# Optimization experiments

Measured on AMD Instinct MI355X. Metric: run time of the kernel, lower is better.

Reference implementation:

```python
import jax, jax.numpy as jnp
import numpy as np

N_NODES = 65536
N_GRAPHS = 32
NODES_PER_GRAPH = 2048
N_EDGES = 1048576
F_IN, H1, H2, OUT = 16, 64, 64, 12


def gcn_conv(x, src, dst, W, b, num_nodes):
    """PyG GCNConv: out = D^{-1/2} (A+I) D^{-1/2} X W + b."""
    loop = jnp.arange(num_nodes, dtype=src.dtype)
    s = jnp.concatenate([src, loop])  # sources incl. self-loops
    d = jnp.concatenate([dst, loop])  # targets incl. self-loops
    deg = jax.ops.segment_sum(jnp.ones_like(d, dtype=x.dtype), d, num_segments=num_nodes)
    dinv = jnp.where(deg > 0, jax.lax.rsqrt(deg), 0.0)
    norm = dinv[s] * dinv[d]  # [E+N]
    h = x @ W  # [N, H]
    msg = h[s] * norm[:, None]  # [E+N, H] -- dominant memory traffic
    return jax.ops.segment_sum(msg, d, num_segments=num_nodes) + b


def setup_inputs() -> dict:
    key = jax.random.key(0)
    k = jax.random.split(key, 8)
    x = jax.random.normal(k[0], (N_NODES, F_IN), dtype=jnp.float32)
    edge_index = jax.random.randint(k[1], (2, N_EDGES), 0, N_NODES, dtype=jnp.int32)
    batch = jnp.repeat(jnp.arange(N_GRAPHS, dtype=jnp.int32), NODES_PER_GRAPH)
    s1 = 1.0 / np.sqrt(F_IN)
    s2 = 1.0 / np.sqrt(H1)
    s3 = 1.0 / np.sqrt(H2 * NODES_PER_GRAPH)
    W1 = jax.random.uniform(k[2], (F_IN, H1), jnp.float32, -s1, s1)
    b1 = jnp.zeros((H1,), jnp.float32)
    W2 = jax.random.uniform(k[3], (H1, H2), jnp.float32, -s2, s2)
    b2 = jnp.zeros((H2,), jnp.float32)
    Wfc = jax.random.uniform(k[4], (H2 * NODES_PER_GRAPH, OUT), jnp.float32, -s3, s3)
    bfc = jax.random.uniform(k[5], (OUT,), jnp.float32, -s3, s3)
    return {"x": x, "edge_index": edge_index, "batch": batch,
            "W1": W1, "b1": b1, "W2": W2, "b2": b2, "Wfc": Wfc, "bfc": bfc}


def reference(x, edge_index, batch, W1, b1, W2, b2, Wfc, bfc):
    src, dst = edge_index[0], edge_index[1]
    h = gcn_conv(x, src, dst, W1, b1, N_NODES)
    h = jnp.tanh(h)  # act1 (dropout rate 0 -> identity)
    h = gcn_conv(h, src, dst, W2, b2, N_NODES)
    h = jnp.tanh(h)  # act2
    # batch is sorted with exactly NODES_PER_GRAPH nodes per graph, so the
    # per-graph masked concat is a reshape: [G, P*H2]
    h_concat = h.reshape(N_GRAPHS, NODES_PER_GRAPH * H2)
    return h_concat @ Wfc + bfc
```

## Files before the change

kernel.cpp:

```cpp
#include <hip/hip_runtime.h>
#include <hip/hip_fp16.h>

#define N_NODES 65536
#define N_EDGES 1048576
#define F_IN    16
#define H       64
#define N_GRAPHS 32
#define NPG     2048
#define OUT_F   12
#define KPG     (NPG * H)
#define CAP     4864
#define NPB     16


__global__ __launch_bounds__(256) void init_kernel(int* __restrict__ gCursor,
                                                   const float* __restrict__ bfc,
                                                   float* __restrict__ out) {
    int t = threadIdx.x;
    gCursor[t] = t * CAP;
    for (int i = t; i < N_GRAPHS * OUT_F; i += 256) out[i] = bfc[i % OUT_F];
}

__global__ __launch_bounds__(256) void binA_kernel(const int* __restrict__ src,
                                                   const int* __restrict__ dst,
                                                   int* __restrict__ gCursor,
                                                   unsigned int* __restrict__ binned) {
    __shared__ int hist[256];
    __shared__ int sc[256];
    __shared__ int bnd[257];
    __shared__ int lcur[256];
    __shared__ int blkBase[256];
    __shared__ unsigned int staged[4096];
    int t = threadIdx.x;
    hist[t] = 0; lcur[t] = 0;
    __syncthreads();
    int e0 = blockIdx.x * 4096;
    unsigned int rec[16];
#pragma unroll
    for (int i = 0; i < 16; i++) {
        int e = e0 + i * 256 + t;
        unsigned int s = (unsigned int)src[e];
        unsigned int d = (unsigned int)dst[e];
        rec[i] = s | (d << 16);
        atomicAdd(&hist[d >> 8], 1);
    }
    __syncthreads();
    int cnt = hist[t];
    if (cnt) blkBase[t] = atomicAdd(&gCursor[t], cnt);
    sc[t] = cnt;
    __syncthreads();
    for (int off = 1; off < 256; off <<= 1) {
        int v = (t >= off) ? sc[t - off] : 0;
        __syncthreads();
        sc[t] += v;
        __syncthreads();
    }
    bnd[t] = sc[t] - cnt;
    if (t == 255) bnd[256] = 4096;
    __syncthreads();
#pragma unroll
    for (int i = 0; i < 16; i++) {
        int b = rec[i] >> 24;
        int p = bnd[b] + atomicAdd(&lcur[b], 1);
        staged[p] = rec[i];
    }
    __syncthreads();
    for (int i = t; i < 4096; i += 256) {
        int lo = 0;
#pragma unroll
        for (int s = 128; s > 0; s >>= 1)
            if (bnd[lo + s] <= i) lo += s;
        binned[blkBase[lo] + (i - bnd[lo])] = staged[i];
    }
}

__global__ __launch_bounds__(256) void binB_g1_kernel(const unsigned int* __restrict__ binned,
                                                      const int* __restrict__ gCursor,
                                                      const float* __restrict__ x,
                                                      int2* __restrict__ rowinfo,
                                                      unsigned short* __restrict__ nbr,
                                                      __half2* __restrict__ g1h) {
    __shared__ int hist[256];
    __shared__ int sc[256];
    __shared__ int off[256];
    __shared__ int cur[256];
    __shared__ unsigned short outS[8192];
    int b = blockIdx.x, t = threadIdx.x;
    int base = b * CAP;
    int cnt  = gCursor[b] - base;
    hist[t] = 0; cur[t] = 0;
    __syncthreads();
    for (int i = t; i < cnt; i += 256) {
        unsigned int r = binned[base + i];
        atomicAdd(&hist[(r >> 16) & 255], 1);
    }
    __syncthreads();
    int c = hist[t];
    sc[t] = c;
    __syncthreads();
    for (int o = 1; o < 256; o <<= 1) {
        int v = (t >= o) ? sc[t - o] : 0;
        __syncthreads();
        sc[t] += v;
        __syncthreads();
    }
    off[t] = sc[t] - c;
    int nd = (b << 8) + t;
    float dv = rsqrtf((float)(c + 1));
    rowinfo[nd] = make_int2(base + sc[t] - c, c);
    {
        const float4* xr = (const float4*)(x + (size_t)nd * F_IN);
        float4 x0 = xr[0], x1 = xr[1], x2 = xr[2], x3 = xr[3];
        __half2* gr = g1h + nd * 8;
        gr[0] = __floats2half2_rn(x0.x * dv, x0.y * dv);
        gr[1] = __floats2half2_rn(x0.z * dv, x0.w * dv);
        gr[2] = __floats2half2_rn(x1.x * dv, x1.y * dv);
        gr[3] = __floats2half2_rn(x1.z * dv, x1.w * dv);
        gr[4] = __floats2half2_rn(x2.x * dv, x2.y * dv);
        gr[5] = __floats2half2_rn(x2.z * dv, x2.w * dv);
        gr[6] = __floats2half2_rn(x3.x * dv, x3.y * dv);
        gr[7] = __floats2half2_rn(x3.z * dv, x3.w * dv);
    }
    __syncthreads();
    for (int i = t; i < cnt; i += 256) {
        unsigned int r = binned[base + i];
        int n = (r >> 16) & 255;
        int p = off[n] + atomicAdd(&cur[n], 1);
        outS[p] = (unsigned short)(r & 0xFFFF);
    }
    __syncthreads();
    for (int i = t; i < cnt; i += 256) nbr[base + i] = outS[i];
}

__device__ __forceinline__ void add8(float* acc, float4 q) {
    union { float4 f; __half2 h[4]; } u; u.f = q;
#pragma unroll
    for (int c = 0; c < 4; c++) {
        float2 p = __half22float2(u.h[c]);
        acc[2 * c]     += p.x;
        acc[2 * c + 1] += p.y;
    }
}
__device__ __forceinline__ void add4(float* acc, float2 q) {
    union { float2 f; __half2 h[2]; } u; u.f = q;
    float2 p0 = __half22float2(u.h[0]);
    float2 p1 = __half22float2(u.h[1]);
    acc[0] += p0.x; acc[1] += p0.y; acc[2] += p1.x; acc[3] += p1.y;
}

__global__ __launch_bounds__(256) void agg1_gemm1_kernel(const __half2* __restrict__ g1h,
                                                         const int2* __restrict__ rowinfo,
                                                         const unsigned short* __restrict__ nbr,
                                                         const float* __restrict__ W1,
                                                         const float* __restrict__ b1,
                                                         __half* __restrict__ g2h) {
    const float2* g1v = (const float2*)g1h;
    __shared__ float Ws[F_IN * H];
    __shared__ float bs[H];
    int t = threadIdx.x;
    for (int i = t; i < F_IN * H; i += 256) Ws[i] = W1[i];
    if (t < H) bs[t] = b1[t];
    __syncthreads();
    int lane = t & 63;
    int w    = t >> 6;
    int f4   = lane & 3;
    int sub  = lane >> 2;
    int v    = blockIdx.x * NPB + w;
    int2 ri  = rowinfo[v];
    int nb   = (int)nbr[ri.x + lane];
#pragma unroll 1
    for (int it = 0; it < NPB / 4; ++it) {
        int vc = v;
        int r0 = ri.x, er = ri.y;
        int nbc = nb;
        float2 sq = g1v[(vc << 2) + f4];
        if (it < NPB / 4 - 1) ri = rowinfo[vc + 4];
        float acc[4] = {0.f, 0.f, 0.f, 0.f};
        int j = 0;
        for (; j + 32 <= er; j += 32) {
            int u0 = __shfl(nbc, j + sub, 64);
            int u1 = __shfl(nbc, j + 16 + sub, 64);
            float2 q0 = g1v[(u0 << 2) + f4];
            float2 q1 = g1v[(u1 << 2) + f4];
            add4(acc, q0);
            add4(acc, q1);
        }
        for (; j < er && j < 64; j += 16) {
            int idx = j + sub;
            int u = __shfl(nbc, idx < er ? idx : 0, 64);
            float2 q = g1v[(u << 2) + f4];
            if (idx < er) add4(acc, q);
        }
        for (int base = 64; base < er; base += 64) {
            int nbx = (int)nbr[r0 + base + lane];
            for (int jj = 0; jj < 64 && base + jj < er; jj += 16) {
                int idx = jj + sub;
                int u = __shfl(nbx, (base + idx) < er ? idx : 0, 64);
                float2 q = g1v[(u << 2) + f4];
                if (base + idx < er) add4(acc, q);
            }
        }
        if (it < NPB / 4 - 1) nb = (int)nbr[ri.x + lane];
#pragma unroll
        for (int i = 0; i < 4; i++) {
            acc[i] += __shfl_xor(acc[i], 4, 64);
            acc[i] += __shfl_xor(acc[i], 8, 64);
            acc[i] += __shfl_xor(acc[i], 16, 64);
            acc[i] += __shfl_xor(acc[i], 32, 64);
        }
        add4(acc, sq);
        float dv = rsqrtf((float)(er + 1));
#pragma unroll
        for (int i = 0; i < 4; i++) acc[i] *= dv;
        float s = bs[lane];
#pragma unroll
        for (int k = 0; k < F_IN; ++k) {
            float bk = __shfl(acc[k & 3], k >> 2, 64);
            s += bk * Ws[k * H + lane];
        }
        g2h[(vc << 6) + lane] = __float2half(dv * tanhf(s));
        v += 4;
    }
}

__global__ __launch_bounds__(256) void agg2_kernel(const __half2* __restrict__ g2h,
                                                   const int2* __restrict__ rowinfo,
                                                   const unsigned short* __restrict__ nbr,
                                                   float* __restrict__ a2) {
    const float4* g2v = (const float4*)g2h;
    int t    = threadIdx.x;
    int lane = t & 63;
    int w    = t >> 6;
    int f8   = lane & 7;
    int sub  = lane >> 3;
    int v    = blockIdx.x * NPB + w;
    int2 ri  = rowinfo[v];
    int nb   = (int)nbr[ri.x + lane];
#pragma unroll 1
    for (int it = 0; it < NPB / 4; ++it) {
        int vc = v;
        int r0 = ri.x, er = ri.y;
        int nbc = nb;
        float4 sq = g2v[(vc << 3) + f8];
        if (it < NPB / 4 - 1) ri = rowinfo[vc + 4];
        float acc[8] = {0.f, 0.f, 0.f, 0.f, 0.f, 0.f, 0.f, 0.f};
        int j = 0;
        for (; j + 16 <= er; j += 16) {
            int u0 = __shfl(nbc, j + sub, 64);
            int u1 = __shfl(nbc, j + 8 + sub, 64);
            float4 q0 = g2v[(u0 << 3) + f8];
            float4 q1 = g2v[(u1 << 3) + f8];
            add8(acc, q0);
            add8(acc, q1);
        }
        for (; j < er && j < 64; j += 8) {
            int idx = j + sub;
            int u = __shfl(nbc, idx < er ? idx : 0, 64);
            float4 q = g2v[(u << 3) + f8];
            if (idx < er) add8(acc, q);
        }
        for (int base = 64; base < er; base += 64) {
            int nbx = (int)nbr[r0 + base + lane];
            for (int jj = 0; jj < 64 && base + jj < er; jj += 8) {
                int idx = jj + sub;
                int u = __shfl(nbx, (base + idx) < er ? idx : 0, 64);
                float4 q = g2v[(u << 3) + f8];
                if (base + idx < er) add8(acc, q);
            }
        }
        if (it < NPB / 4 - 1) nb = (int)nbr[ri.x + lane];
#pragma unroll
        for (int i = 0; i < 8; i++) {
            acc[i] += __shfl_xor(acc[i], 8, 64);
            acc[i] += __shfl_xor(acc[i], 16, 64);
            acc[i] += __shfl_xor(acc[i], 32, 64);
        }
        add8(acc, sq);
        float dv = rsqrtf((float)(er + 1));
#pragma unroll
        for (int i = 0; i < 8; i++) acc[i] *= dv;
        if (sub == 0) {
            float4* dp = (float4*)(a2 + ((size_t)vc << 6) + (f8 << 3));
            dp[0] = make_float4(acc[0], acc[1], acc[2], acc[3]);
            dp[1] = make_float4(acc[4], acc[5], acc[6], acc[7]);
        }
        v += 4;
    }
}

__global__ __launch_bounds__(256) void gemm2_fc_kernel(const float* __restrict__ a2,
                                                       const float* __restrict__ W2,
                                                       const float* __restrict__ b2,
                                                       const float* __restrict__ Wfc,
                                                       float* __restrict__ out) {
    __shared__ float Ws[H * H];
    __shared__ float As[64 * H];
    __shared__ float bs[H];
    __shared__ float red[4][OUT_F];
    int t = threadIdx.x;
    for (int i = t; i < H * H; i += 256) Ws[i] = W2[i];
    if (t < H) bs[t] = b2[t];
    {
        const float4* ap = (const float4*)(a2 + ((size_t)blockIdx.x << 12));
        float4* asp = (float4*)As;
#pragma unroll
        for (int i = 0; i < 4; i++) asp[i * 256 + t] = ap[i * 256 + t];
    }
    __syncthreads();
    int lane = t & 63, w = t >> 6;
    int v0 = blockIdx.x * 64 + (w << 4);
    int g  = blockIdx.x >> 5;
    float acc[16];
#pragma unroll
    for (int j = 0; j < 16; j++) acc[j] = bs[lane];
    const float* asBase = As + ((w << 4) * H);
#pragma unroll 2
    for (int kc = 0; kc < H / 4; ++kc) {
        int k0 = kc << 2;
        float w0 = Ws[(k0 + 0) * H + lane];
        float w1 = Ws[(k0 + 1) * H + lane];
        float w2 = Ws[(k0 + 2) * H + lane];
        float w3 = Ws[(k0 + 3) * H + lane];
#pragma unroll
        for (int j = 0; j < 16; ++j) {
            float4 aq = *(const float4*)(asBase + j * H + k0);
            acc[j] += aq.x * w0 + aq.y * w1 + aq.z * w2 + aq.w * w3;
        }
    }
    float pa[OUT_F];
#pragma unroll
    for (int j = 0; j < OUT_F; j++) pa[j] = 0.f;
#pragma unroll
    for (int j = 0; j < 16; ++j) {
        float hv = tanhf(acc[j]);
        int vl = (v0 + j) & (NPG - 1);
        const float4* wr = (const float4*)(Wfc + (size_t)(vl * H + lane) * OUT_F);
        float4 q0 = wr[0], q1 = wr[1], q2 = wr[2];
        pa[0]  += hv * q0.x;  pa[1]  += hv * q0.y;
        pa[2]  += hv * q0.z;  pa[3]  += hv * q0.w;
        pa[4]  += hv * q1.x;  pa[5]  += hv * q1.y;
        pa[6]  += hv * q1.z;  pa[7]  += hv * q1.w;
        pa[8]  += hv * q2.x;  pa[9]  += hv * q2.y;
        pa[10] += hv * q2.z;  pa[11] += hv * q2.w;
    }
#pragma unroll
    for (int j = 0; j < OUT_F; j++) {
        float vv = pa[j];
        vv += __shfl_xor(vv, 1, 64);  vv += __shfl_xor(vv, 2, 64);
        vv += __shfl_xor(vv, 4, 64);  vv += __shfl_xor(vv, 8, 64);
        vv += __shfl_xor(vv, 16, 64); vv += __shfl_xor(vv, 32, 64);
        pa[j] = vv;
    }
    if (lane == 0) {
#pragma unroll
        for (int j = 0; j < OUT_F; j++) red[w][j] = pa[j];
    }
    __syncthreads();
    if (t < OUT_F)
        atomicAdd(&out[g * OUT_F + t], red[0][t] + red[1][t] + red[2][t] + red[3][t]);
}

extern "C" void kernel_launch(void* const* d_in, const int* in_sizes, int n_in,
                              void* d_out, int out_size, void* d_ws, size_t ws_size,
                              hipStream_t stream) {
    const float* x    = (const float*)d_in[0];
    const int*   edge = (const int*)d_in[1];
    const int*   src  = edge;
    const int*   dst  = edge + N_EDGES;
    const float* W1  = (const float*)d_in[3];
    const float* b1  = (const float*)d_in[4];
    const float* W2  = (const float*)d_in[5];
    const float* b2  = (const float*)d_in[6];
    const float* Wfc = (const float*)d_in[7];
    const float* bfc = (const float*)d_in[8];
    float* out = (float*)d_out;

    char* p = (char*)d_ws;
    auto alloc = [&](size_t n) { char* r = p; p += (n + 255) & ~(size_t)255; return r; };
    int*   gCursor    = (int*)alloc(256 * 4);
    int2*  rowinfo    = (int2*)alloc((size_t)N_NODES * 8);
    unsigned short* nbr = (unsigned short*)alloc((size_t)256 * CAP * 2 + 256);
    __half* g1h       = (__half*)alloc((size_t)N_NODES * F_IN * 2);
    __half* g2h       = (__half*)alloc((size_t)N_NODES * H * 2);
    float* a2         = (float*)alloc((size_t)N_NODES * H * 4);
    unsigned int* binned = (unsigned int*)alloc((size_t)256 * CAP * 4);

    init_kernel<<<1, 256, 0, stream>>>(gCursor, bfc, out);
    binA_kernel<<<256, 256, 0, stream>>>(src, dst, gCursor, binned);
    binB_g1_kernel<<<256, 256, 0, stream>>>(binned, gCursor, x, rowinfo, nbr,
                                            (__half2*)g1h);
    agg1_gemm1_kernel<<<N_NODES / NPB, 256, 0, stream>>>((const __half2*)g1h, rowinfo, nbr,
                                                         W1, b1, g2h);
    agg2_kernel<<<N_NODES / NPB, 256, 0, stream>>>((const __half2*)g2h, rowinfo, nbr, a2);
    gemm2_fc_kernel<<<N_NODES / 64, 256, 0, stream>>>(a2, W2, b2, Wfc, out);
}
```

Measured before the change: 187.0 us.

## Split agg1 and GEMM1, prefetch first neighbor gathers, simplify bin scatter

The fused layer-1 aggregation and GEMM becomes two kernels. agg1 writes the normalized 16-feature aggregate to a new fp32 buffer, and a separate register-blocked gemm1 kernel applies W1, bias, tanh and the degree scale. Both aggregation kernels now issue their first neighbor gathers before the rowinfo prefetch so more loads are in flight. binA reads the bucket from each staged record instead of binary-searching the boundaries. This trades an extra kernel launch and an extra 4 MB round trip for less shuffle work per node and more memory-level parallelism.

```diff
diff --git a/kernel.cpp b/kernel.cpp
--- a/kernel.cpp
+++ b/kernel.cpp
@@ -27,7 +27,7 @@
                                                    unsigned int* __restrict__ binned) {
     __shared__ int hist[256];
     __shared__ int sc[256];
-    __shared__ int bnd[257];
+    __shared__ int bnd[256];
     __shared__ int lcur[256];
     __shared__ int blkBase[256];
     __shared__ unsigned int staged[4096];
@@ -56,7 +56,6 @@
         __syncthreads();
     }
     bnd[t] = sc[t] - cnt;
-    if (t == 255) bnd[256] = 4096;
     __syncthreads();
 #pragma unroll
     for (int i = 0; i < 16; i++) {
@@ -66,11 +65,9 @@
     }
     __syncthreads();
     for (int i = t; i < 4096; i += 256) {
-        int lo = 0;
-#pragma unroll
-        for (int s = 128; s > 0; s >>= 1)
-            if (bnd[lo + s] <= i) lo += s;
-        binned[blkBase[lo] + (i - bnd[lo])] = staged[i];
+        unsigned int r = staged[i];
+        int b = r >> 24;
+        binned[blkBase[b] + (i - bnd[b])] = r;
     }
 }
 
@@ -148,19 +145,12 @@
     acc[0] += p0.x; acc[1] += p0.y; acc[2] += p1.x; acc[3] += p1.y;
 }
 
-__global__ __launch_bounds__(256) void agg1_gemm1_kernel(const __half2* __restrict__ g1h,
-                                                         const int2* __restrict__ rowinfo,
-                                                         const unsigned short* __restrict__ nbr,
-                                                         const float* __restrict__ W1,
-                                                         const float* __restrict__ b1,
-                                                         __half* __restrict__ g2h) {
+__global__ __launch_bounds__(256) void agg1_kernel(const __half2* __restrict__ g1h,
+                                                   const int2* __restrict__ rowinfo,
+                                                   const unsigned short* __restrict__ nbr,
+                                                   float* __restrict__ a1) {
     const float2* g1v = (const float2*)g1h;
-    __shared__ float Ws[F_IN * H];
-    __shared__ float bs[H];
-    int t = threadIdx.x;
-    for (int i = t; i < F_IN * H; i += 256) Ws[i] = W1[i];
-    if (t < H) bs[t] = b1[t];
-    __syncthreads();
+    int t    = threadIdx.x;
     int lane = t & 63;
     int w    = t >> 6;
     int f4   = lane & 3;
@@ -174,16 +164,23 @@
         int r0 = ri.x, er = ri.y;
         int nbc = nb;
         float2 sq = g1v[(vc << 2) + f4];
+        int s0 = sub, s1 = 16 + sub;
+        int u0 = __shfl(nbc, s0 < er ? s0 : 0, 64);
+        int u1 = __shfl(nbc, s1 < er ? s1 : 0, 64);
+        float2 q0 = g1v[(u0 << 2) + f4];
+        float2 q1 = g1v[(u1 << 2) + f4];
         if (it < NPB / 4 - 1) ri = rowinfo[vc + 4];
         float acc[4] = {0.f, 0.f, 0.f, 0.f};
-        int j = 0;
+        if (s0 < er) add4(acc, q0);
+        if (s1 < er) add4(acc, q1);
+        int j = 32;
         for (; j + 32 <= er; j += 32) {
-            int u0 = __shfl(nbc, j + sub, 64);
-            int u1 = __shfl(nbc, j + 16 + sub, 64);
-            float2 q0 = g1v[(u0 << 2) + f4];
-            float2 q1 = g1v[(u1 << 2) + f4];
-            add4(acc, q0);
-            add4(acc, q1);
+            int a0 = __shfl(nbc, j + sub, 64);
+            int a1i = __shfl(nbc, j + 16 + sub, 64);
+            float2 t0 = g1v[(a0 << 2) + f4];
+            float2 t1 = g1v[(a1i << 2) + f4];
+            add4(acc, t0);
+            add4(acc, t1);
         }
         for (; j < er && j < 64; j += 16) {
             int idx = j + sub;
@@ -210,16 +207,56 @@
         }
         add4(acc, sq);
         float dv = rsqrtf((float)(er + 1));
-#pragma unroll
-        for (int i = 0; i < 4; i++) acc[i] *= dv;
-        float s = bs[lane];
-#pragma unroll
-        for (int k = 0; k < F_IN; ++k) {
-            float bk = __shfl(acc[k & 3], k >> 2, 64);
-            s += bk * Ws[k * H + lane];
-        }
-        g2h[(vc << 6) + lane] = __float2half(dv * tanhf(s));
+        if (sub == 0) {
+            float4* dp = (float4*)(a1 + ((size_t)vc << 4) + (f4 << 2));
+            dp[0] = make_float4(dv * acc[0], dv * acc[1], dv * acc[2], dv * acc[3]);
+        }
         v += 4;
+    }
+}
+
+__global__ __launch_bounds__(256) void gemm1_kernel(const float* __restrict__ a1,
+                                                    const int2* __restrict__ rowinfo,
+                                                    const float* __restrict__ W1,
+                                                    const float* __restrict__ b1,
+                                                    __half* __restrict__ g2h) {
+    __shared__ float Ws[F_IN * H];
+    __shared__ float As[64 * F_IN];
+    __shared__ float bs[H];
+    __shared__ float degs[64];
+    int t = threadIdx.x;
+    for (int i = t; i < F_IN * H; i += 256) Ws[i] = W1[i];
+    if (t < H) bs[t] = b1[t];
+    int v0 = blockIdx.x * 64;
+    if (t < 64) degs[t] = (float)(rowinfo[v0 + t].y + 1);
+    {
+        const float4* ap = (const float4*)(a1 + ((size_t)v0 << 4));
+        ((float4*)As)[t] = ap[t];
+    }
+    __syncthreads();
+    int lane = t & 63, w = t >> 6;
+    float acc[16];
+#pragma unroll
+    for (int j = 0; j < 16; j++) acc[j] = bs[lane];
+    const float* asBase = As + ((w << 4) * F_IN);
+#pragma unroll
+    for (int kc = 0; kc < F_IN / 4; ++kc) {
+        int k0 = kc << 2;
+        float w0 = Ws[(k0 + 0) * H + lane];
+        float w1 = Ws[(k0 + 1) * H + lane];
+        float w2 = Ws[(k0 + 2) * H + lane];
+        float w3 = Ws[(k0 + 3) * H + lane];
+#pragma unroll
+        for (int j = 0; j < 16; ++j) {
+            float4 aq = *(const float4*)(asBase + j * F_IN + k0);
+            acc[j] += aq.x * w0 + aq.y * w1 + aq.z * w2 + aq.w * w3;
+        }
+    }
+    int vw = v0 + (w << 4);
+#pragma unroll
+    for (int j = 0; j < 16; ++j) {
+        float dv = rsqrtf(degs[(w << 4) + j]);
+        g2h[((size_t)(vw + j) << 6) + lane] = __float2half(dv * tanhf(acc[j]));
     }
 }
 
@@ -242,16 +279,29 @@
         int r0 = ri.x, er = ri.y;
         int nbc = nb;
         float4 sq = g2v[(vc << 3) + f8];
+        int s0 = sub, s1 = 8 + sub, s2 = 16 + sub, s3 = 24 + sub;
+        int u0 = __shfl(nbc, s0 < er ? s0 : 0, 64);
+        int u1 = __shfl(nbc, s1 < er ? s1 : 0, 64);
+        int u2 = __shfl(nbc, s2 < er ? s2 : 0, 64);
+        int u3 = __shfl(nbc, s3 < er ? s3 : 0, 64);
+        float4 q0 = g2v[(u0 << 3) + f8];
+        float4 q1 = g2v[(u1 << 3) + f8];
+        float4 q2 = g2v[(u2 << 3) + f8];
+        float4 q3 = g2v[(u3 << 3) + f8];
         if (it < NPB / 4 - 1) ri = rowinfo[vc + 4];
         float acc[8] = {0.f, 0.f, 0.f, 0.f, 0.f, 0.f, 0.f, 0.f};
-        int j = 0;
-        for (; j + 16 <= er; j += 16) {
-            int u0 = __shfl(nbc, j + sub, 64);
-            int u1 = __shfl(nbc, j + 8 + sub, 64);
-            float4 q0 = g2v[(u0 << 3) + f8];
-            float4 q1 = g2v[(u1 << 3) + f8];
-            add8(acc, q0);
-            add8(acc, q1);
+        if (s0 < er) add8(acc, q0);
+        if (s1 < er) add8(acc, q1);
+        if (s2 < er) add8(acc, q2);
+        if (s3 < er) add8(acc, q3);
+        int j = 32;
+        for (; j + 16 <= er && j < 64; j += 16) {
+            int a0 = __shfl(nbc, j + sub, 64);
+            int a1i = __shfl(nbc, j + 8 + sub, 64);
+            float4 t0 = g2v[(a0 << 3) + f8];
+            float4 t1 = g2v[(a1i << 3) + f8];
+            add8(acc, t0);
+            add8(acc, t1);
         }
         for (; j < er && j < 64; j += 8) {
             int idx = j + sub;
@@ -381,6 +431,7 @@
     int2*  rowinfo    = (int2*)alloc((size_t)N_NODES * 8);
     unsigned short* nbr = (unsigned short*)alloc((size_t)256 * CAP * 2 + 256);
     __half* g1h       = (__half*)alloc((size_t)N_NODES * F_IN * 2);
+    float* a1         = (float*)alloc((size_t)N_NODES * F_IN * 4);
     __half* g2h       = (__half*)alloc((size_t)N_NODES * H * 2);
     float* a2         = (float*)alloc((size_t)N_NODES * H * 4);
     unsigned int* binned = (unsigned int*)alloc((size_t)256 * CAP * 4);
@@ -389,8 +440,8 @@
     binA_kernel<<<256, 256, 0, stream>>>(src, dst, gCursor, binned);
     binB_g1_kernel<<<256, 256, 0, stream>>>(binned, gCursor, x, rowinfo, nbr,
                                             (__half2*)g1h);
-    agg1_gemm1_kernel<<<N_NODES / NPB, 256, 0, stream>>>((const __half2*)g1h, rowinfo, nbr,
-                                                         W1, b1, g2h);
+    agg1_kernel<<<N_NODES / NPB, 256, 0, stream>>>((const __half2*)g1h, rowinfo, nbr, a1);
+    gemm1_kernel<<<N_NODES / 64, 256, 0, stream>>>(a1, rowinfo, W1, b1, g2h);
     agg2_kernel<<<N_NODES / NPB, 256, 0, stream>>>((const __half2*)g2h, rowinfo, nbr, a2);
     gemm2_fc_kernel<<<N_NODES / 64, 256, 0, stream>>>(a2, W2, b2, Wfc, out);
 }
```

Measured after the change: 188.5 us. Within noise of the previous version (+0.8%).
